# Performance work log

Hardware: AMD Instinct MI355X
Metric: run time of the kernel (lower is better)

## Reference

```python
import jax, jax.numpy as jnp
import numpy as np

B, T, V, F = 32, 128, 128, 64
K_ORDER = 3
N_FILT = 64

def setup_inputs() -> dict:
    key = jax.random.key(0)
    k1, k2, k3 = jax.random.split(key, 3)
    x = jax.random.normal(k1, (B, T, V, F), dtype=jnp.float32)
    W = jax.random.uniform(k2, (B, V, V), dtype=jnp.float32)  # learned adjacency, nonneg
    # keras 'uniform' initializer default range [-0.05, 0.05]
    Theta = jax.random.uniform(k3, (K_ORDER, F, N_FILT), dtype=jnp.float32, minval=-0.05, maxval=0.05)
    return {"x": x, "W": W, "Theta": Theta}

def reference(x, W, Theta):
    # x: (B,T,V,F), W: (B,V,V), Theta: (k,F,O)
    k = Theta.shape[0]
    v = x.shape[2]
    eye = jnp.eye(v, dtype=x.dtype)
    deg = jnp.sum(W, axis=1)                      # (B,V) -- sum over axis=1 as in K.sum(W, axis=1)
    D = eye[None, :, :] * deg[:, :, None]         # matrix_diag(deg)
    L = D - W
    L_t = L - eye[None, :, :]                     # 2*L/lambda_max - I with lambda_max=2
    chebs = [jnp.broadcast_to(eye[None, :, :], W.shape), L_t]
    for i in range(2, k):
        # NOTE: elementwise multiply, faithful to the original tf code (tf `*`)
        chebs.append(2.0 * L_t * chebs[-1] - chebs[-2])
    Tk = jnp.stack(chebs, axis=0)                 # (k,B,V,V)
    # out[b,t,u,o] = sum_{k,v,f} Tk[k,b,v,u] * x[b,t,v,f] * Theta[k,f,o]
    # (T_k transposed matmul graph_signal, then dot with theta_k, summed over k and t-batched)
    out = jnp.einsum('kbvu,btvf,kfo->btuo', Tk, x, Theta)
    return jax.nn.relu(out)
```

## Files before the change

### kernel.cpp

```cpp
#include <hip/hip_runtime.h>

typedef __attribute__((ext_vector_type(8))) short bf16x8;
typedef __attribute__((ext_vector_type(4))) float f32x4;

namespace {

constexpr int B = 32, T = 128, V = 128, F = 64, O = 64;

constexpr size_t WS_THT_OFF = (size_t)B * V * 256 * 2;
constexpr size_t WS_LDG_OFF = WS_THT_OFF + 192 * 64 * 2;

__device__ inline unsigned short f2bf(float f) {
    unsigned u = __builtin_bit_cast(unsigned, f);
    u += 0x7FFFu + ((u >> 16) & 1u);
    return (unsigned short)(u >> 16);
}

__global__ __launch_bounds__(256) void prep(const float* __restrict__ W,
                                            const float* __restrict__ Theta,
                                            unsigned short* __restrict__ acat,
                                            unsigned short* __restrict__ tht,
                                            float* __restrict__ ldg) {
    const int tid = threadIdx.x;
    if (blockIdx.x == B) {
        for (int i = 0; i < 192 * 64 / 256; ++i) {
            int idx = tid + i * 256;
            int n = idx >> 6, f = idx & 63;
            float v;
            if (n < 64)       v = Theta[f * 64 + n] - Theta[2 * 4096 + f * 64 + n];
            else if (n < 128) v = Theta[4096 + f * 64 + (n - 64)];
            else              v = Theta[2 * 4096 + f * 64 + (n - 128)];
            tht[idx] = f2bf(v);
        }
        return;
    }
    const int b = blockIdx.x;
    const float* Wb = W + (size_t)b * V * V;
    __shared__ float Wl[V][V + 1];
    for (int i = 0; i < V * V / 256; ++i) {
        int idx = tid + i * 256;
        Wl[idx >> 7][idx & 127] = Wb[idx];
    }
    __syncthreads();
    if (tid < V) {
        float s = 0.f;
        for (int i = 0; i < V; ++i) s += Wl[i][tid];
        ldg[b * V + tid] = s - 1.0f - Wl[tid][tid];
    }
    unsigned short* ab = acat + (size_t)b * V * 256;
    for (int i = 0; i < V; ++i) {
        int idx = tid + i * 256;
        int u = idx >> 8, kv = idx & 255, v = kv & 127;
        float wv = Wl[v][u];
        float val = (v == u) ? 0.f : ((kv < 128) ? -wv : 2.f * wv * wv);
        ab[idx] = f2bf(val);
    }
}

__global__ __launch_bounds__(256, 3) void graph_conv_main(
    const float* __restrict__ x, const unsigned short* __restrict__ acat,
    const unsigned short* __restrict__ tht_g, const float* __restrict__ ldg,
    float* __restrict__ out) {
    const int t = blockIdx.x, b = blockIdx.y;
    const int tid = threadIdx.x;
    const int lane = tid & 63, w = tid >> 6;
    const int lr = lane & 15, lg = lane >> 4;

    __shared__ __align__(16) unsigned short smem[20480];
    __shared__ __align__(16) float ldg_s[V];
    unsigned short* xs = smem;
    unsigned short* th = smem + 8192;
    unsigned short* zct = smem;

    const float* xbt = x + ((size_t)(b * T + t)) * (V * F);
#pragma unroll
    for (int i = 0; i < 4; ++i) {
        int c = tid + i * 256;
        int row = c >> 3, c8 = c & 7;
        const float4* p = (const float4*)(xbt + row * 64 + c8 * 8);
        float4 q0 = p[0], q1 = p[1];
        uint4 val;
        val.x = f2bf(q0.x) | ((unsigned)f2bf(q0.y) << 16);
        val.y = f2bf(q0.z) | ((unsigned)f2bf(q0.w) << 16);
        val.z = f2bf(q1.x) | ((unsigned)f2bf(q1.y) << 16);
        val.w = f2bf(q1.z) | ((unsigned)f2bf(q1.w) << 16);
        int off = row * 128 + ((c8 * 16) ^ ((row & 7) << 4));
        *(uint4*)((char*)xs + off) = val;
    }
#pragma unroll
    for (int i = 0; i < 6; ++i) {
        int c = tid + i * 256;
        int row = c >> 3, c8 = c & 7;
        uint4 val = *(const uint4*)(tht_g + row * 64 + c8 * 8);
        int off = row * 128 + ((c8 * 16) ^ ((row & 7) << 4));
        *(uint4*)((char*)th + off) = val;
    }
    if (tid < V) ldg_s[tid] = ldg[b * V + tid];
    __syncthreads();

    f32x4 acc[2][4];
    f32x4 z[2][8];
#pragma unroll
    for (int vf = 0; vf < 2; ++vf) {
#pragma unroll
        for (int of = 0; of < 4; ++of) acc[vf][of] = (f32x4){0.f, 0.f, 0.f, 0.f};
#pragma unroll
        for (int nf = 0; nf < 8; ++nf) z[vf][nf] = (f32x4){0.f, 0.f, 0.f, 0.f};
    }
#pragma unroll
    for (int ks = 0; ks < 2; ++ks) {
        bf16x8 xa[2];
#pragma unroll
        for (int vf = 0; vf < 2; ++vf) {
            int row = w * 32 + 16 * vf + lr;
            int off = row * 128 + ((ks * 64 + lg * 16) ^ ((row & 7) << 4));
            xa[vf] = *(const bf16x8*)((const char*)xs + off);
        }
#pragma unroll
        for (int nf = 0; nf < 12; ++nf) {
            int rowt = nf * 16 + lr;
            int off = rowt * 128 + ((ks * 64 + lg * 16) ^ ((rowt & 7) << 4));
            bf16x8 tb = *(const bf16x8*)((const char*)th + off);
            if (nf < 4) {
                acc[0][nf] = __builtin_amdgcn_mfma_f32_16x16x32_bf16(xa[0], tb, acc[0][nf], 0, 0, 0);
                acc[1][nf] = __builtin_amdgcn_mfma_f32_16x16x32_bf16(xa[1], tb, acc[1][nf], 0, 0, 0);
            } else {
                z[0][nf - 4] = __builtin_amdgcn_mfma_f32_16x16x32_bf16(xa[0], tb, z[0][nf - 4], 0, 0, 0);
                z[1][nf - 4] = __builtin_amdgcn_mfma_f32_16x16x32_bf16(xa[1], tb, z[1][nf - 4], 0, 0, 0);
            }
        }
    }

#pragma unroll
    for (int vf = 0; vf < 2; ++vf) {
        f32x4 ld = *(const f32x4*)(ldg_s + w * 32 + 16 * vf + lg * 4);
        f32x4 ld2 = 2.0f * ld * ld;
#pragma unroll
        for (int of = 0; of < 4; ++of)
            acc[vf][of] += ld * z[vf][of] + ld2 * z[vf][4 + of];
    }

    __syncthreads();

#pragma unroll
    for (int vf = 0; vf < 2; ++vf) {
        int vcol = w * 32 + 16 * vf + lg * 4;
#pragma unroll
        for (int of = 0; of < 4; ++of) {
            int rowz = of * 16 + lr;
            f32x4 z1 = z[vf][of], z2 = z[vf][4 + of];
            uint2 q1, q2;
            q1.x = f2bf(z1[0]) | ((unsigned)f2bf(z1[1]) << 16);
            q1.y = f2bf(z1[2]) | ((unsigned)f2bf(z1[3]) << 16);
            q2.x = f2bf(z2[0]) | ((unsigned)f2bf(z2[1]) << 16);
            q2.y = f2bf(z2[2]) | ((unsigned)f2bf(z2[3]) << 16);
            int base = rowz * 512;
            *(uint2*)((char*)zct + base + (((vcol * 2)) ^ ((rowz & 7) << 4))) = q1;
            *(uint2*)((char*)zct + base + ((256 + vcol * 2) ^ ((rowz & 7) << 4))) = q2;
        }
    }
    __syncthreads();

    const unsigned short* ab = acat + (size_t)b * V * 256;
#pragma unroll
    for (int ks = 0; ks < 8; ++ks) {
        bf16x8 af[2];
#pragma unroll
        for (int uf = 0; uf < 2; ++uf) {
            int rowa = w * 32 + 16 * uf + lr;
            af[uf] = *(const bf16x8*)(ab + rowa * 256 + ks * 32 + lg * 8);
        }
#pragma unroll
        for (int of = 0; of < 4; ++of) {
            int rowz = of * 16 + lr;
            int off = rowz * 512 + ((ks * 64 + lg * 16) ^ ((rowz & 7) << 4));
            bf16x8 zb = *(const bf16x8*)((const char*)zct + off);
            acc[0][of] = __builtin_amdgcn_mfma_f32_16x16x32_bf16(af[0], zb, acc[0][of], 0, 0, 0);
            acc[1][of] = __builtin_amdgcn_mfma_f32_16x16x32_bf16(af[1], zb, acc[1][of], 0, 0, 0);
        }
    }

    float* obt = out + ((size_t)(b * T + t)) * (V * O);
#pragma unroll
    for (int vf = 0; vf < 2; ++vf)
#pragma unroll
        for (int of = 0; of < 4; ++of)
#pragma unroll
            for (int j = 0; j < 4; ++j) {
                int u = w * 32 + 16 * vf + lg * 4 + j;
                int o = of * 16 + lr;
                float r = acc[vf][of][j];
                obt[u * 64 + o] = r > 0.f ? r : 0.f;
            }
}

}

extern "C" void kernel_launch(void* const* d_in, const int* in_sizes, int n_in,
                              void* d_out, int out_size, void* d_ws, size_t ws_size,
                              hipStream_t stream) {
    const float* x = (const float*)d_in[0];
    const float* W = (const float*)d_in[1];
    const float* Theta = (const float*)d_in[2];
    float* outp = (float*)d_out;

    unsigned short* acat = (unsigned short*)d_ws;
    unsigned short* tht = (unsigned short*)((char*)d_ws + WS_THT_OFF);
    float* ldg = (float*)((char*)d_ws + WS_LDG_OFF);

    prep<<<B + 1, 256, 0, stream>>>(W, Theta, acat, tht, ldg);
    graph_conv_main<<<dim3(T, B), 256, 0, stream>>>(x, acat, tht, ldg, outp);
}
```

Before: 81.14 us.

## Process four timesteps per block with register prefetch of next x slice

Each block now handles four consecutive timesteps, loading Theta and degree terms into shared memory once and reusing them across all four. The next timestep's x slice is prefetched into registers while the current one is computed, then converted to bf16 and stored in shared memory after the z staging. Shared buffers are split instead of aliased, and launch bounds drop from 3 to 2 blocks per SM. The aim is to hide global load latency and amortise setup, at the cost of fewer blocks, lower occupancy and more register pressure from the prefetch.

```diff
diff --git a/kernel.cpp b/kernel.cpp
--- a/kernel.cpp
+++ b/kernel.cpp
@@ -6,6 +6,7 @@
 namespace {
 
 constexpr int B = 32, T = 128, V = 128, F = 64, O = 64;
+constexpr int TPB = 4;
 
 constexpr size_t WS_THT_OFF = (size_t)B * V * 256 * 2;
 constexpr size_t WS_LDG_OFF = WS_THT_OFF + 192 * 64 * 2;
@@ -57,36 +58,26 @@
     }
 }
 
-__global__ __launch_bounds__(256, 3) void graph_conv_main(
+__global__ __launch_bounds__(256, 2) void graph_conv_main(
     const float* __restrict__ x, const unsigned short* __restrict__ acat,
     const unsigned short* __restrict__ tht_g, const float* __restrict__ ldg,
     float* __restrict__ out) {
-    const int t = blockIdx.x, b = blockIdx.y;
+    const int t0 = blockIdx.x * TPB, b = blockIdx.y;
     const int tid = threadIdx.x;
     const int lane = tid & 63, w = tid >> 6;
     const int lr = lane & 15, lg = lane >> 4;
 
-    __shared__ __align__(16) unsigned short smem[20480];
+    __shared__ __align__(16) unsigned short th[192 * 64];
+    __shared__ __align__(16) unsigned short xs[V * F];
+    __shared__ __align__(16) unsigned short zct[64 * 256];
     __shared__ __align__(16) float ldg_s[V];
-    unsigned short* xs = smem;
-    unsigned short* th = smem + 8192;
-    unsigned short* zct = smem;
-
-    const float* xbt = x + ((size_t)(b * T + t)) * (V * F);
-#pragma unroll
-    for (int i = 0; i < 4; ++i) {
-        int c = tid + i * 256;
-        int row = c >> 3, c8 = c & 7;
-        const float4* p = (const float4*)(xbt + row * 64 + c8 * 8);
-        float4 q0 = p[0], q1 = p[1];
-        uint4 val;
-        val.x = f2bf(q0.x) | ((unsigned)f2bf(q0.y) << 16);
-        val.y = f2bf(q0.z) | ((unsigned)f2bf(q0.w) << 16);
-        val.z = f2bf(q1.x) | ((unsigned)f2bf(q1.y) << 16);
-        val.w = f2bf(q1.z) | ((unsigned)f2bf(q1.w) << 16);
-        int off = row * 128 + ((c8 * 16) ^ ((row & 7) << 4));
-        *(uint4*)((char*)xs + off) = val;
-    }
+
+    const float* xb = x + ((size_t)(b * T + t0)) * (V * F);
+
+    float4 pf[8];
+#pragma unroll
+    for (int i = 0; i < 8; ++i) pf[i] = ((const float4*)xb)[tid + i * 256];
+
 #pragma unroll
     for (int i = 0; i < 6; ++i) {
         int c = tid + i * 256;
@@ -96,102 +87,133 @@
         *(uint4*)((char*)th + off) = val;
     }
     if (tid < V) ldg_s[tid] = ldg[b * V + tid];
+
+#pragma unroll
+    for (int i = 0; i < 8; ++i) {
+        int p = tid + i * 256;
+        int row = p >> 4, c4 = p & 15;
+        uint2 q;
+        q.x = f2bf(pf[i].x) | ((unsigned)f2bf(pf[i].y) << 16);
+        q.y = f2bf(pf[i].z) | ((unsigned)f2bf(pf[i].w) << 16);
+        *(uint2*)((char*)xs + row * 128 + ((c4 * 8) ^ ((row & 7) << 4))) = q;
+    }
     __syncthreads();
 
-    f32x4 acc[2][4];
-    f32x4 z[2][8];
-#pragma unroll
-    for (int vf = 0; vf < 2; ++vf) {
-#pragma unroll
-        for (int of = 0; of < 4; ++of) acc[vf][of] = (f32x4){0.f, 0.f, 0.f, 0.f};
-#pragma unroll
-        for (int nf = 0; nf < 8; ++nf) z[vf][nf] = (f32x4){0.f, 0.f, 0.f, 0.f};
-    }
-#pragma unroll
-    for (int ks = 0; ks < 2; ++ks) {
-        bf16x8 xa[2];
+    const unsigned short* ab = acat + (size_t)b * V * 256;
+
+    for (int tt = 0; tt < TPB; ++tt) {
+        if (tt + 1 < TPB) {
+            const float4* nxt = (const float4*)(xb + (size_t)(tt + 1) * (V * F));
+#pragma unroll
+            for (int i = 0; i < 8; ++i) pf[i] = nxt[tid + i * 256];
+        }
+
+        f32x4 acc[2][4];
+        f32x4 z[2][8];
 #pragma unroll
         for (int vf = 0; vf < 2; ++vf) {
-            int row = w * 32 + 16 * vf + lr;
-            int off = row * 128 + ((ks * 64 + lg * 16) ^ ((row & 7) << 4));
-            xa[vf] = *(const bf16x8*)((const char*)xs + off);
-        }
-#pragma unroll
-        for (int nf = 0; nf < 12; ++nf) {
-            int rowt = nf * 16 + lr;
-            int off = rowt * 128 + ((ks * 64 + lg * 16) ^ ((rowt & 7) << 4));
-            bf16x8 tb = *(const bf16x8*)((const char*)th + off);
-            if (nf < 4) {
-                acc[0][nf] = __builtin_amdgcn_mfma_f32_16x16x32_bf16(xa[0], tb, acc[0][nf], 0, 0, 0);
-                acc[1][nf] = __builtin_amdgcn_mfma_f32_16x16x32_bf16(xa[1], tb, acc[1][nf], 0, 0, 0);
-            } else {
-                z[0][nf - 4] = __builtin_amdgcn_mfma_f32_16x16x32_bf16(xa[0], tb, z[0][nf - 4], 0, 0, 0);
-                z[1][nf - 4] = __builtin_amdgcn_mfma_f32_16x16x32_bf16(xa[1], tb, z[1][nf - 4], 0, 0, 0);
-            }
-        }
-    }
-
-#pragma unroll
-    for (int vf = 0; vf < 2; ++vf) {
-        f32x4 ld = *(const f32x4*)(ldg_s + w * 32 + 16 * vf + lg * 4);
-        f32x4 ld2 = 2.0f * ld * ld;
-#pragma unroll
-        for (int of = 0; of < 4; ++of)
-            acc[vf][of] += ld * z[vf][of] + ld2 * z[vf][4 + of];
-    }
-
-    __syncthreads();
-
-#pragma unroll
-    for (int vf = 0; vf < 2; ++vf) {
-        int vcol = w * 32 + 16 * vf + lg * 4;
-#pragma unroll
-        for (int of = 0; of < 4; ++of) {
-            int rowz = of * 16 + lr;
-            f32x4 z1 = z[vf][of], z2 = z[vf][4 + of];
-            uint2 q1, q2;
-            q1.x = f2bf(z1[0]) | ((unsigned)f2bf(z1[1]) << 16);
-            q1.y = f2bf(z1[2]) | ((unsigned)f2bf(z1[3]) << 16);
-            q2.x = f2bf(z2[0]) | ((unsigned)f2bf(z2[1]) << 16);
-            q2.y = f2bf(z2[2]) | ((unsigned)f2bf(z2[3]) << 16);
-            int base = rowz * 512;
-            *(uint2*)((char*)zct + base + (((vcol * 2)) ^ ((rowz & 7) << 4))) = q1;
-            *(uint2*)((char*)zct + base + ((256 + vcol * 2) ^ ((rowz & 7) << 4))) = q2;
-        }
-    }
-    __syncthreads();
-
-    const unsigned short* ab = acat + (size_t)b * V * 256;
-#pragma unroll
-    for (int ks = 0; ks < 8; ++ks) {
-        bf16x8 af[2];
-#pragma unroll
-        for (int uf = 0; uf < 2; ++uf) {
-            int rowa = w * 32 + 16 * uf + lr;
-            af[uf] = *(const bf16x8*)(ab + rowa * 256 + ks * 32 + lg * 8);
-        }
-#pragma unroll
-        for (int of = 0; of < 4; ++of) {
-            int rowz = of * 16 + lr;
-            int off = rowz * 512 + ((ks * 64 + lg * 16) ^ ((rowz & 7) << 4));
-            bf16x8 zb = *(const bf16x8*)((const char*)zct + off);
-            acc[0][of] = __builtin_amdgcn_mfma_f32_16x16x32_bf16(af[0], zb, acc[0][of], 0, 0, 0);
-            acc[1][of] = __builtin_amdgcn_mfma_f32_16x16x32_bf16(af[1], zb, acc[1][of], 0, 0, 0);
-        }
-    }
-
-    float* obt = out + ((size_t)(b * T + t)) * (V * O);
-#pragma unroll
-    for (int vf = 0; vf < 2; ++vf)
-#pragma unroll
-        for (int of = 0; of < 4; ++of)
-#pragma unroll
-            for (int j = 0; j < 4; ++j) {
-                int u = w * 32 + 16 * vf + lg * 4 + j;
-                int o = of * 16 + lr;
-                float r = acc[vf][of][j];
-                obt[u * 64 + o] = r > 0.f ? r : 0.f;
-            }
+#pragma unroll
+            for (int of = 0; of < 4; ++of) acc[vf][of] = (f32x4){0.f, 0.f, 0.f, 0.f};
+#pragma unroll
+            for (int nf = 0; nf < 8; ++nf) z[vf][nf] = (f32x4){0.f, 0.f, 0.f, 0.f};
+        }
+#pragma unroll
+        for (int ks = 0; ks < 2; ++ks) {
+            bf16x8 xa[2];
+#pragma unroll
+            for (int vf = 0; vf < 2; ++vf) {
+                int row = w * 32 + 16 * vf + lr;
+                int off = row * 128 + ((ks * 64 + lg * 16) ^ ((row & 7) << 4));
+                xa[vf] = *(const bf16x8*)((const char*)xs + off);
+            }
+#pragma unroll
+            for (int nf = 0; nf < 12; ++nf) {
+                int rowt = nf * 16 + lr;
+                int off = rowt * 128 + ((ks * 64 + lg * 16) ^ ((rowt & 7) << 4));
+                bf16x8 tb = *(const bf16x8*)((const char*)th + off);
+                if (nf < 4) {
+                    acc[0][nf] = __builtin_amdgcn_mfma_f32_16x16x32_bf16(xa[0], tb, acc[0][nf], 0, 0, 0);
+                    acc[1][nf] = __builtin_amdgcn_mfma_f32_16x16x32_bf16(xa[1], tb, acc[1][nf], 0, 0, 0);
+                } else {
+                    z[0][nf - 4] = __builtin_amdgcn_mfma_f32_16x16x32_bf16(xa[0], tb, z[0][nf - 4], 0, 0, 0);
+                    z[1][nf - 4] = __builtin_amdgcn_mfma_f32_16x16x32_bf16(xa[1], tb, z[1][nf - 4], 0, 0, 0);
+                }
+            }
+        }
+
+#pragma unroll
+        for (int vf = 0; vf < 2; ++vf) {
+            f32x4 ld = *(const f32x4*)(ldg_s + w * 32 + 16 * vf + lg * 4);
+            f32x4 ld2 = 2.0f * ld * ld;
+#pragma unroll
+            for (int of = 0; of < 4; ++of)
+                acc[vf][of] += ld * z[vf][of] + ld2 * z[vf][4 + of];
+        }
+
+        __syncthreads();
+
+#pragma unroll
+        for (int vf = 0; vf < 2; ++vf) {
+            int vcol = w * 32 + 16 * vf + lg * 4;
+#pragma unroll
+            for (int of = 0; of < 4; ++of) {
+                int rowz = of * 16 + lr;
+                f32x4 z1 = z[vf][of], z2 = z[vf][4 + of];
+                uint2 q1, q2;
+                q1.x = f2bf(z1[0]) | ((unsigned)f2bf(z1[1]) << 16);
+                q1.y = f2bf(z1[2]) | ((unsigned)f2bf(z1[3]) << 16);
+                q2.x = f2bf(z2[0]) | ((unsigned)f2bf(z2[1]) << 16);
+                q2.y = f2bf(z2[2]) | ((unsigned)f2bf(z2[3]) << 16);
+                int base = rowz * 512;
+                *(uint2*)((char*)zct + base + (((vcol * 2)) ^ ((rowz & 7) << 4))) = q1;
+                *(uint2*)((char*)zct + base + ((256 + vcol * 2) ^ ((rowz & 7) << 4))) = q2;
+            }
+        }
+
+        if (tt + 1 < TPB) {
+#pragma unroll
+            for (int i = 0; i < 8; ++i) {
+                int p = tid + i * 256;
+                int row = p >> 4, c4 = p & 15;
+                uint2 q;
+                q.x = f2bf(pf[i].x) | ((unsigned)f2bf(pf[i].y) << 16);
+                q.y = f2bf(pf[i].z) | ((unsigned)f2bf(pf[i].w) << 16);
+                *(uint2*)((char*)xs + row * 128 + ((c4 * 8) ^ ((row & 7) << 4))) = q;
+            }
+        }
+        __syncthreads();
+
+#pragma unroll
+        for (int ks = 0; ks < 8; ++ks) {
+            bf16x8 af[2];
+#pragma unroll
+            for (int uf = 0; uf < 2; ++uf) {
+                int rowa = w * 32 + 16 * uf + lr;
+                af[uf] = *(const bf16x8*)(ab + rowa * 256 + ks * 32 + lg * 8);
+            }
+#pragma unroll
+            for (int of = 0; of < 4; ++of) {
+                int rowz = of * 16 + lr;
+                int off = rowz * 512 + ((ks * 64 + lg * 16) ^ ((rowz & 7) << 4));
+                bf16x8 zb = *(const bf16x8*)((const char*)zct + off);
+                acc[0][of] = __builtin_amdgcn_mfma_f32_16x16x32_bf16(af[0], zb, acc[0][of], 0, 0, 0);
+                acc[1][of] = __builtin_amdgcn_mfma_f32_16x16x32_bf16(af[1], zb, acc[1][of], 0, 0, 0);
+            }
+        }
+
+        float* obt = out + ((size_t)(b * T + t0 + tt)) * (V * O);
+#pragma unroll
+        for (int vf = 0; vf < 2; ++vf)
+#pragma unroll
+            for (int of = 0; of < 4; ++of)
+#pragma unroll
+                for (int j = 0; j < 4; ++j) {
+                    int u = w * 32 + 16 * vf + lg * 4 + j;
+                    int o = of * 16 + lr;
+                    float r = acc[vf][of][j];
+                    obt[u * 64 + o] = r > 0.f ? r : 0.f;
+                }
+    }
 }
 
 }
@@ -209,5 +231,5 @@
     float* ldg = (float*)((char*)d_ws + WS_LDG_OFF);
 
     prep<<<B + 1, 256, 0, stream>>>(W, Theta, acat, tht, ldg);
-    graph_conv_main<<<dim3(T, B), 256, 0, stream>>>(x, acat, tht, ldg, outp);
-}
+    graph_conv_main<<<dim3(T / TPB, B), 256, 0, stream>>>(x, acat, tht, ldg, outp);
+}
```

After: 174.4 us. 2.15x slower.
